# Kernel tuning notes

Hardware: AMD Instinct MI355X
Metric: run time of the kernel (lower is better)

Reference implementation:

```python
import jax, jax.numpy as jnp
import numpy as np

# Static configuration (matches init_kwargs)
L = 3264          # seq_length
K = 12            # ktc=4 -> K=12
LOCC = 4          # ktc=4 -> Locc=4
S, B, A = 8, 64, 4  # streams (user/port pairs), batch, rx antennas
DELAY_MIN, DELAY_MAX = -10, 10


def _phasor(m):
    # m: integer shifts [S, B] -> exp(1j*2*pi*m*n/L) as [S, B, L]
    n = jnp.arange(L, dtype=jnp.int32)
    ang = (2.0 * np.pi / L) * ((m[..., None] * n) % L).astype(jnp.float32)
    return jax.lax.complex(jnp.cos(ang), jnp.sin(ang))


def _linear_interp(h_avg):
    # np.interp with uniform source grid orig[i] = (LOCC-1)/2 + i*LOCC, clamped at ends.
    # h_avg: [S, B, A, R] complex, R = L // LOCC -> [S, B, A, L]
    R = L // LOCC
    new = jnp.arange(L, dtype=jnp.float32)
    t = jnp.clip((new - (LOCC - 1) / 2.0) / LOCC, 0.0, float(R - 1))
    i0 = jnp.floor(t).astype(jnp.int32)
    i1 = jnp.minimum(i0 + 1, R - 1)
    frac = (t - i0).astype(jnp.float32)
    return h_avg[..., i0] * (1.0 - frac) + h_avg[..., i1] * frac


def reference(ls_real, ls_imag, cyclic_shifts, noise_powers):
    ls = jax.lax.complex(ls_real, ls_imag)                     # [S,B,A,L]
    ideal_peak = ((K - cyclic_shifts) % K) * (L // K)          # [S]

    # Stage 1: IFFT + timing-offset search (torch.no_grad in original)
    h_time = jnp.fft.ifft(ls, axis=-1)
    power = jax.lax.stop_gradient(jnp.sum(jnp.abs(h_time) ** 2, axis=2))  # [S,B,L]
    offs = jnp.arange(DELAY_MIN, DELAY_MAX + 1, dtype=jnp.int32)          # [21]
    cand_idx = (ideal_peak[:, None] + offs[None, :]) % L                   # [S,21]
    cand_idx = jnp.broadcast_to(cand_idx[:, None, :], (S, B, offs.shape[0]))
    cand_pow = jnp.take_along_axis(power, cand_idx, axis=-1)               # [S,B,21]
    t_off = offs[jnp.argmax(cand_pow, axis=-1)]                            # [S,B]
    m = t_off + ideal_peak[:, None]                                        # [S,B]
    ph_m = _phasor(m)        # [S,B,L]
    ph_T = _phasor(t_off)    # [S,B,L]

    # Stage 2: phasor shift, OCC demux, interpolation (inside no_grad in original)
    h_shift = ls * ph_m[:, :, None, :]
    h_avg = h_shift.reshape(S, B, A, L // LOCC, LOCC).mean(-1)             # [S,B,A,L/4]
    h_interp = jax.lax.stop_gradient(_linear_interp(h_avg))                # [S,B,A,L]

    # Stage 3: global residual against stream (0,0)'s LS estimate
    total_recon = jnp.sum(h_interp * jnp.conj(ph_m)[:, :, None, :], axis=0)  # [B,A,L]
    residual = ls[0] - total_recon                                           # [B,A,L]

    # Stage 4: apply residual, MMSE (identity: mmse_module=None), timing recovery
    h_wr = h_interp + residual[None, :, :, None, :].squeeze(3) if False else h_interp + residual[None] * ph_m[:, :, None, :]
    final = h_wr * jnp.conj(ph_T)[:, :, None, :]                             # [S,B,A,L]
    return jnp.stack([final.real, final.imag]).astype(jnp.float32)          # [2,S,B,A,L]


def setup_inputs() -> dict:
    key = jax.random.key(0)
    k1, k2, k3, k4 = jax.random.split(key, 4)
    return {
        "ls_real": jax.random.normal(k1, (S, B, A, L), dtype=jnp.float32),
        "ls_imag": jax.random.normal(k2, (S, B, A, L), dtype=jnp.float32),
        "cyclic_shifts": jax.random.randint(k3, (S,), 0, K, dtype=jnp.int32),
        "noise_powers": jax.random.uniform(k4, (B,), dtype=jnp.float32),
    }
```

## Files before the change

### kernel.cpp

```cpp
#include <hip/hip_runtime.h>

namespace {

constexpr int L = 3264;
constexpr int K = 12;
constexpr int S = 8;
constexpr int B = 64;
constexpr int A = 4;
constexpr int R = 816;
constexpr int NOFF = 21;
constexpr int PEAK_STEP = L / K;
constexpr float TWO_PI = 6.28318530717958647692f;
constexpr int NCHUNK = (L + 255) / 256;

__global__ __launch_bounds__(512)
void k_stage1(const float* __restrict__ lsr, const float* __restrict__ lsi,
              const int* __restrict__ cs,
              int* __restrict__ toff_out, int* __restrict__ m_out,
              float2* __restrict__ havg)
{
    __shared__ float2 red[8][NOFF];
    __shared__ int m_sh;

    const int sb = blockIdx.x;
    const int s = sb >> 6;
    const int tid = threadIdx.x;
    const int lane = tid & 63;
    const int w = tid >> 6;
    const int a = w >> 1;
    const int h = w & 1;

    const int csv = cs[s];
    const int ideal = ((K - csv) % K) * PEAK_STEP;
    int idx0 = (ideal - 10) % L; if (idx0 < 0) idx0 += L;

    const size_t rowbase = ((size_t)sb * A + a) * L;
    const float* __restrict__ pr = lsr + rowbase;
    const float* __restrict__ pi = lsi + rowbase;

    float ar[NOFF], ai[NOFF];
    #pragma unroll
    for (int d = 0; d < NOFF; ++d) { ar[d] = 0.f; ai[d] = 0.f; }

    for (int k = h * 64 + lane; k < L; k += 128) {
        const float xr = pr[k];
        const float xi = pi[k];
        const int j0 = (k * idx0) % L;
        float wr, wi, str, sti;
        __sincosf((TWO_PI / (float)L) * (float)j0, &wi, &wr);
        __sincosf((TWO_PI / (float)L) * (float)k,  &sti, &str);
        #pragma unroll
        for (int d = 0; d < NOFF; ++d) {
            ar[d] += xr * wr - xi * wi;
            ai[d] += xr * wi + xi * wr;
            const float nwr = wr * str - wi * sti;
            wi = wr * sti + wi * str;
            wr = nwr;
        }
    }

    #pragma unroll
    for (int d = 0; d < NOFF; ++d) {
        float r = ar[d], im = ai[d];
        #pragma unroll
        for (int o = 32; o > 0; o >>= 1) {
            r  += __shfl_xor(r, o);
            im += __shfl_xor(im, o);
        }
        if (lane == 0) red[w][d] = make_float2(r, im);
    }
    __syncthreads();

    if (w == 0) {
        float pw = -1.f;
        if (lane < NOFF) {
            pw = 0.f;
            #pragma unroll
            for (int a2 = 0; a2 < A; ++a2) {
                const float2 u = red[2 * a2][lane];
                const float2 v = red[2 * a2 + 1][lane];
                const float rr = u.x + v.x;
                const float ii = u.y + v.y;
                pw += rr * rr + ii * ii;
            }
        }
        float mx = pw;
        #pragma unroll
        for (int o = 32; o > 0; o >>= 1) mx = fmaxf(mx, __shfl_xor(mx, o));
        const unsigned long long msk = __ballot(pw == mx);
        const int argd = __ffsll(msk) - 1;
        if (lane == 0) {
            const int toff = argd - 10;
            toff_out[sb] = toff;
            m_out[sb]    = toff + ideal;
            m_sh         = toff + ideal;
        }
    }
    __syncthreads();

    int mp = m_sh % L; if (mp < 0) mp += L;
    float smr, smi;
    __sincosf((TWO_PI / (float)L) * (float)mp, &smi, &smr);

    for (int aa = 0; aa < A; ++aa) {
        const float* __restrict__ qr = lsr + ((size_t)sb * A + aa) * L;
        const float* __restrict__ qi = lsi + ((size_t)sb * A + aa) * L;
        float2* __restrict__ dst = havg + ((size_t)sb * A + aa) * R;
        for (int i = tid; i < R; i += 512) {
            const int l0 = 4 * i;
            int j = (mp * l0) % L;
            float wr2, wi2;
            __sincosf((TWO_PI / (float)L) * (float)j, &wi2, &wr2);
            float are = 0.f, aim = 0.f;
            #pragma unroll
            for (int jj = 0; jj < 4; ++jj) {
                const float xr = qr[l0 + jj];
                const float xi = qi[l0 + jj];
                are += xr * wr2 - xi * wi2;
                aim += xr * wi2 + xi * wr2;
                const float nw = wr2 * smr - wi2 * smi;
                wi2 = wr2 * smi + wi2 * smr;
                wr2 = nw;
            }
            dst[i] = make_float2(are * 0.25f, aim * 0.25f);
        }
    }
}

__global__ __launch_bounds__(256)
void k_final(const float* __restrict__ lsr, const float* __restrict__ lsi,
             const int* __restrict__ toff_arr, const int* __restrict__ m_arr,
             const float2* __restrict__ havg,
             float* __restrict__ out)
{
    const int bid = blockIdx.x;
    const int chunk = bid % NCHUNK;
    const int ba = bid / NCHUNK;
    const int b = ba >> 2;
    const int a = ba & 3;
    const int l = chunk * 256 + (int)threadIdx.x;
    if (l >= L) return;

    float t = ((float)l - 1.5f) * 0.25f;
    t = fminf(fmaxf(t, 0.0f), (float)(R - 1));
    const int i0 = (int)t;
    const int i1 = min(i0 + 1, R - 1);
    const float frac = t - (float)i0;

    float hire[S], hiim[S], pmre[S], pmim[S];
    float rre = 0.f, rim = 0.f;

    #pragma unroll
    for (int s = 0; s < S; ++s) {
        const int sb = s * B + b;
        int mp = m_arr[sb] % L; if (mp < 0) mp += L;
        const int j = (mp * l) % L;
        float sv, cv;
        __sincosf((TWO_PI / (float)L) * (float)j, &sv, &cv);
        const float2 h0 = havg[((size_t)sb * A + a) * R + i0];
        const float2 h1 = havg[((size_t)sb * A + a) * R + i1];
        const float hr = h0.x * (1.f - frac) + h1.x * frac;
        const float hi = h0.y * (1.f - frac) + h1.y * frac;
        hire[s] = hr; hiim[s] = hi; pmre[s] = cv; pmim[s] = sv;
        rre += hr * cv + hi * sv;
        rim += hi * cv - hr * sv;
    }

    const size_t off0 = ((size_t)(b * A + a)) * L + l;
    const float resre = lsr[off0] - rre;
    const float resim = lsi[off0] - rim;

    #pragma unroll
    for (int s = 0; s < S; ++s) {
        const float wre = hire[s] + resre * pmre[s] - resim * pmim[s];
        const float wim = hiim[s] + resre * pmim[s] + resim * pmre[s];
        int jt = (toff_arr[s * B + b] * l) % L; if (jt < 0) jt += L;
        float sv, cv;
        __sincosf((TWO_PI / (float)L) * (float)jt, &sv, &cv);
        const float fre = wre * cv + wim * sv;
        const float fim = wim * cv - wre * sv;
        const size_t o = (((size_t)(s * B + b)) * A + a) * L + l;
        __builtin_nontemporal_store(fre, &out[o]);
        __builtin_nontemporal_store(fim, &out[(size_t)S * B * A * L + o]);
    }
}

}

extern "C" void kernel_launch(void* const* d_in, const int* in_sizes, int n_in,
                              void* d_out, int out_size, void* d_ws, size_t ws_size,
                              hipStream_t stream) {
    (void)in_sizes; (void)n_in; (void)out_size; (void)ws_size;
    const float* lsr = (const float*)d_in[0];
    const float* lsi = (const float*)d_in[1];
    const int*   cs  = (const int*)d_in[2];

    int* toff = (int*)d_ws;
    int* marr = toff + 512;
    float2* havg = (float2*)((char*)d_ws + 4096);

    k_stage1<<<S * B, 512, 0, stream>>>(lsr, lsi, cs, toff, marr, havg);
    k_final<<<B * A * NCHUNK, 256, 0, stream>>>(lsr, lsi, toff, marr, havg,
                                                (float*)d_out);
}
```

Measured before the change: 173.9 us.

## Replace per-element sincos with twiddle table and precomputed phasor recurrences

Adds a small kernel that builds a cos/sin twiddle table of length L, which the stage-1 demux and the final kernel then look up instead of calling sincos per element. The stage-1 timing search now precomputes per-lane starting phasors and wave-uniform stride phasors, so its inner loop has no sincos or modulo. The demux loads use float4. The aim is to cut transcendental and integer-modulo work; in exchange there is an extra launch, gather loads from the table, and possible drift in accuracy from the long phasor recurrences.

```diff
diff --git a/kernel.cpp b/kernel.cpp
--- a/kernel.cpp
+++ b/kernel.cpp
@@ -11,11 +11,27 @@
 constexpr int NOFF = 21;
 constexpr int PEAK_STEP = L / K;
 constexpr float TWO_PI = 6.28318530717958647692f;
+constexpr float CINV = TWO_PI / (float)L;
 constexpr int NCHUNK = (L + 255) / 256;
+
+__device__ __forceinline__ float rfl(float x) {
+    return __uint_as_float(__builtin_amdgcn_readfirstlane(__float_as_uint(x)));
+}
+
+__global__ __launch_bounds__(256)
+void k_table(float2* __restrict__ tw)
+{
+    const int j = blockIdx.x * 256 + threadIdx.x;
+    if (j < L) {
+        float sv, cv;
+        __sincosf(CINV * (float)j, &sv, &cv);
+        tw[j] = make_float2(cv, sv);
+    }
+}
 
 __global__ __launch_bounds__(512)
 void k_stage1(const float* __restrict__ lsr, const float* __restrict__ lsi,
-              const int* __restrict__ cs,
+              const int* __restrict__ cs, const float2* __restrict__ tw,
               int* __restrict__ toff_out, int* __restrict__ m_out,
               float2* __restrict__ havg)
 {
@@ -34,28 +50,61 @@
     const int ideal = ((K - csv) % K) * PEAK_STEP;
     int idx0 = (ideal - 10) % L; if (idx0 < 0) idx0 += L;
 
+    const int k0 = h * 64 + lane;
+
+    const int jb = (k0 * idx0) % L;
+    float br, bi; __sincosf(CINV * (float)jb, &bi, &br);
+    float lr, li; __sincosf(CINV * (float)k0, &li, &lr);
+    float pwr[NOFF], pwi[NOFF];
+    pwr[0] = br; pwi[0] = bi;
+    #pragma unroll
+    for (int d = 1; d < NOFF; ++d) {
+        pwr[d] = pwr[d-1] * lr - pwi[d-1] * li;
+        pwi[d] = pwr[d-1] * li + pwi[d-1] * lr;
+    }
+
+    const int js = (128 * idx0) % L;
+    float s0r, s0i; __sincosf(CINV * (float)js, &s0i, &s0r);
+    float e8r, e8i; __sincosf(CINV * 128.0f, &e8i, &e8r);
+    float str_[NOFF], sti_[NOFF];
+    {
+        float cr = s0r, ci = s0i;
+        #pragma unroll
+        for (int d = 0; d < NOFF; ++d) {
+            str_[d] = rfl(cr); sti_[d] = rfl(ci);
+            const float nr = cr * e8r - ci * e8i;
+            ci = cr * e8i + ci * e8r;
+            cr = nr;
+        }
+    }
+
     const size_t rowbase = ((size_t)sb * A + a) * L;
     const float* __restrict__ pr = lsr + rowbase;
-    const float* __restrict__ pi = lsi + rowbase;
+    const float* __restrict__ pi_ = lsi + rowbase;
 
     float ar[NOFF], ai[NOFF];
     #pragma unroll
     for (int d = 0; d < NOFF; ++d) { ar[d] = 0.f; ai[d] = 0.f; }
 
-    for (int k = h * 64 + lane; k < L; k += 128) {
-        const float xr = pr[k];
-        const float xi = pi[k];
-        const int j0 = (k * idx0) % L;
-        float wr, wi, str, sti;
-        __sincosf((TWO_PI / (float)L) * (float)j0, &wi, &wr);
-        __sincosf((TWO_PI / (float)L) * (float)k,  &sti, &str);
+    for (int it = 0; it < 25; ++it) {
+        const float xr = pr[k0 + (it << 7)];
+        const float xi = pi_[k0 + (it << 7)];
         #pragma unroll
         for (int d = 0; d < NOFF; ++d) {
-            ar[d] += xr * wr - xi * wi;
-            ai[d] += xr * wi + xi * wr;
-            const float nwr = wr * str - wi * sti;
-            wi = wr * sti + wi * str;
-            wr = nwr;
+            ar[d] += xr * pwr[d] - xi * pwi[d];
+            ai[d] += xr * pwi[d] + xi * pwr[d];
+            const float nr = pwr[d] * str_[d] - pwi[d] * sti_[d];
+            pwi[d] = pwr[d] * sti_[d] + pwi[d] * str_[d];
+            pwr[d] = nr;
+        }
+    }
+    if (k0 < 64) {
+        const float xr = pr[k0 + 3200];
+        const float xi = pi_[k0 + 3200];
+        #pragma unroll
+        for (int d = 0; d < NOFF; ++d) {
+            ar[d] += xr * pwr[d] - xi * pwi[d];
+            ai[d] += xr * pwi[d] + xi * pwr[d];
         }
     }
 
@@ -99,29 +148,26 @@
     __syncthreads();
 
     int mp = m_sh % L; if (mp < 0) mp += L;
-    float smr, smi;
-    __sincosf((TWO_PI / (float)L) * (float)mp, &smi, &smr);
+    const float2 emp = tw[mp];
 
     for (int aa = 0; aa < A; ++aa) {
-        const float* __restrict__ qr = lsr + ((size_t)sb * A + aa) * L;
-        const float* __restrict__ qi = lsi + ((size_t)sb * A + aa) * L;
+        const float4* __restrict__ qr4 = (const float4*)(lsr + ((size_t)sb * A + aa) * L);
+        const float4* __restrict__ qi4 = (const float4*)(lsi + ((size_t)sb * A + aa) * L);
         float2* __restrict__ dst = havg + ((size_t)sb * A + aa) * R;
         for (int i = tid; i < R; i += 512) {
-            const int l0 = 4 * i;
-            int j = (mp * l0) % L;
-            float wr2, wi2;
-            __sincosf((TWO_PI / (float)L) * (float)j, &wi2, &wr2);
-            float are = 0.f, aim = 0.f;
-            #pragma unroll
-            for (int jj = 0; jj < 4; ++jj) {
-                const float xr = qr[l0 + jj];
-                const float xi = qi[l0 + jj];
-                are += xr * wr2 - xi * wi2;
-                aim += xr * wi2 + xi * wr2;
-                const float nw = wr2 * smr - wi2 * smi;
-                wi2 = wr2 * smi + wi2 * smr;
-                wr2 = nw;
-            }
+            const int j = (mp * (4 * i)) % L;
+            const float2 w0 = tw[j];
+            const float4 xr = qr4[i];
+            const float4 xi = qi4[i];
+            float wr = w0.x, wi = w0.y;
+            float are, aim, nr;
+            are  = xr.x * wr - xi.x * wi;  aim  = xr.x * wi + xi.x * wr;
+            nr = wr * emp.x - wi * emp.y;  wi = wr * emp.y + wi * emp.x;  wr = nr;
+            are += xr.y * wr - xi.y * wi;  aim += xr.y * wi + xi.y * wr;
+            nr = wr * emp.x - wi * emp.y;  wi = wr * emp.y + wi * emp.x;  wr = nr;
+            are += xr.z * wr - xi.z * wi;  aim += xr.z * wi + xi.z * wr;
+            nr = wr * emp.x - wi * emp.y;  wi = wr * emp.y + wi * emp.x;  wr = nr;
+            are += xr.w * wr - xi.w * wi;  aim += xr.w * wi + xi.w * wr;
             dst[i] = make_float2(are * 0.25f, aim * 0.25f);
         }
     }
@@ -130,7 +176,7 @@
 __global__ __launch_bounds__(256)
 void k_final(const float* __restrict__ lsr, const float* __restrict__ lsi,
              const int* __restrict__ toff_arr, const int* __restrict__ m_arr,
-             const float2* __restrict__ havg,
+             const float2* __restrict__ havg, const float2* __restrict__ tw,
              float* __restrict__ out)
 {
     const int bid = blockIdx.x;
@@ -154,16 +200,14 @@
     for (int s = 0; s < S; ++s) {
         const int sb = s * B + b;
         int mp = m_arr[sb] % L; if (mp < 0) mp += L;
-        const int j = (mp * l) % L;
-        float sv, cv;
-        __sincosf((TWO_PI / (float)L) * (float)j, &sv, &cv);
+        const float2 wm = tw[(mp * l) % L];
         const float2 h0 = havg[((size_t)sb * A + a) * R + i0];
         const float2 h1 = havg[((size_t)sb * A + a) * R + i1];
         const float hr = h0.x * (1.f - frac) + h1.x * frac;
         const float hi = h0.y * (1.f - frac) + h1.y * frac;
-        hire[s] = hr; hiim[s] = hi; pmre[s] = cv; pmim[s] = sv;
-        rre += hr * cv + hi * sv;
-        rim += hi * cv - hr * sv;
+        hire[s] = hr; hiim[s] = hi; pmre[s] = wm.x; pmim[s] = wm.y;
+        rre += hr * wm.x + hi * wm.y;
+        rim += hi * wm.x - hr * wm.y;
     }
 
     const size_t off0 = ((size_t)(b * A + a)) * L + l;
@@ -175,10 +219,9 @@
         const float wre = hire[s] + resre * pmre[s] - resim * pmim[s];
         const float wim = hiim[s] + resre * pmim[s] + resim * pmre[s];
         int jt = (toff_arr[s * B + b] * l) % L; if (jt < 0) jt += L;
-        float sv, cv;
-        __sincosf((TWO_PI / (float)L) * (float)jt, &sv, &cv);
-        const float fre = wre * cv + wim * sv;
-        const float fim = wim * cv - wre * sv;
+        const float2 wt = tw[jt];
+        const float fre = wre * wt.x + wim * wt.y;
+        const float fim = wim * wt.x - wre * wt.y;
         const size_t o = (((size_t)(s * B + b)) * A + a) * L + l;
         __builtin_nontemporal_store(fre, &out[o]);
         __builtin_nontemporal_store(fim, &out[(size_t)S * B * A * L + o]);
@@ -197,9 +240,11 @@
 
     int* toff = (int*)d_ws;
     int* marr = toff + 512;
-    float2* havg = (float2*)((char*)d_ws + 4096);
-
-    k_stage1<<<S * B, 512, 0, stream>>>(lsr, lsi, cs, toff, marr, havg);
-    k_final<<<B * A * NCHUNK, 256, 0, stream>>>(lsr, lsi, toff, marr, havg,
+    float2* tw = (float2*)((char*)d_ws + 4096);
+    float2* havg = (float2*)((char*)d_ws + 36864);
+
+    k_table<<<NCHUNK, 256, 0, stream>>>(tw);
+    k_stage1<<<S * B, 512, 0, stream>>>(lsr, lsi, cs, tw, toff, marr, havg);
+    k_final<<<B * A * NCHUNK, 256, 0, stream>>>(lsr, lsi, toff, marr, havg, tw,
                                                 (float*)d_out);
 }
```

Measured after the change: 180.8 us. +4.0%, slower.
